# Performance work log

Measured on AMD Instinct MI355X. Metric: run time of the kernel, lower is better.

The kernel has to match this reference:

```python
import jax, jax.numpy as jnp
import numpy as np

N, E, CIN, A, C, NB, B = 20000, 100000, 64, 32, 256, 4, 128
FD = C * NB  # fusion_dims = channels + c_growth*(n_blocks_out-1) with c_growth==channels
HID = 1024


def setup_inputs() -> dict:
    key = jax.random.key(0)
    ks = jax.random.split(key, 24)
    s = 0.05
    inp = {
        "x": jax.random.normal(ks[0], (N, CIN), jnp.float32),
        "edges": jax.random.randint(ks[1], (2, E), 0, N, jnp.int32),
        "edge_weights": jax.random.uniform(ks[2], (E,), jnp.float32),
        "edge_attrs": jax.random.normal(ks[3], (E, A), jnp.float32),
        "bbox_idx": jax.random.randint(ks[4], (N,), 0, B, jnp.int32),
        "num_boxes": B,
        # head GraphConv params: message MLP on [x_dst, x_src-x_dst, edge_attr]
        "W_msg0": jax.random.normal(ks[5], (2 * CIN + A, C), jnp.float32) * s,
        "b_msg0": jnp.zeros((C,), jnp.float32),
        "W_sup0": jax.random.normal(ks[6], (C + CIN, C), jnp.float32) * s,
        "b_sup0": jnp.zeros((C,), jnp.float32),
        # ResBlock params (n_blocks-1 blocks)
        "W_msg": jax.random.normal(ks[7], (NB - 1, 2 * C + A, C), jnp.float32) * s,
        "b_msg": jnp.zeros((NB - 1, C), jnp.float32),
        "W_sup": jax.random.normal(ks[8], (NB - 1, 2 * C, C), jnp.float32) * s,
        "b_sup": jnp.zeros((NB - 1, C), jnp.float32),
        # fusion MLPs [fusion_dims -> 1024]
        "W_fuse": jax.random.normal(ks[9], (FD, HID), jnp.float32) * s,
        "b_fuse": jnp.zeros((HID,), jnp.float32),
        "W_fuse_sup": jax.random.normal(ks[10], (FD, HID), jnp.float32) * s,
        "b_fuse_sup": jnp.zeros((HID,), jnp.float32),
    }
    return inp


def reference(x, edge_weights, edge_attrs, W_msg0, b_msg0, W_sup0, b_sup0,
              W_msg, b_msg, W_sup, b_sup, W_fuse, b_fuse, W_fuse_sup, b_fuse_sup,
              edges, bbox_idx, num_boxes):
    src, dst = edges[0], edges[1]
    n = x.shape[0]

    def gconv(f_in, Wm, bm):
        # per-edge message on [f_dst, f_src - f_dst, edge_attr], weighted sum-aggregate to dst
        h = jnp.concatenate([f_in[dst], f_in[src] - f_in[dst], edge_attrs], axis=1)
        m = jax.nn.relu(h @ Wm + bm) * edge_weights[:, None]
        return jax.ops.segment_sum(m, dst, num_segments=n)

    def super_node(f, x_node, Ws, bs):
        return jax.nn.relu(jnp.concatenate([f, x_node], axis=1) @ Ws + bs)

    # head GraphConv
    f = gconv(x, W_msg0, b_msg0)
    fs = super_node(f, x, W_sup0, b_sup0)
    feats, feats_super = [f], [fs]
    # ResBlocks: residual on node features, fresh super features
    for i in range(NB - 1):
        f = gconv(feats[-1], W_msg[i], b_msg[i]) + feats[-1]
        fs = super_node(f, feats_super[-1], W_sup[i], b_sup[i])
        feats.append(f)
        feats_super.append(fs)

    # n_blocks_out == n_blocks -> take all blocks
    feats_cat = jnp.concatenate(feats, axis=1)            # [N, FD]
    fusion = jax.nn.relu(feats_cat @ W_fuse + b_fuse)     # [N, 1024]
    out_feat = jnp.concatenate([fusion, feats_cat], axis=1)

    fs_cat = jnp.concatenate(feats_super, axis=1)         # [N, FD]
    sums = jax.ops.segment_sum(fs_cat, bbox_idx, num_segments=num_boxes)
    cnts = jax.ops.segment_sum(jnp.ones((n, 1), fs_cat.dtype), bbox_idx, num_segments=num_boxes)
    fs_mean = sums / jnp.maximum(cnts, 1.0)               # scatter(reduce='mean')
    fusion_sup = jax.nn.relu(fs_mean @ W_fuse_sup + b_fuse_sup)
    out_feat_super = jnp.concatenate([fusion_sup, fs_mean], axis=1)
    return out_feat, out_feat_super
```

## Files before the change

kernel.cpp:

```cpp
#include <hip/hip_runtime.h>

#define N_NODES 20000
#define N_EDGES 100000
#define CIN     64
#define A_DIM   32
#define CCH     256
#define NBOX    128
#define FD      1024
#define HID     1024
#define OUT_STRIDE 2048

typedef __attribute__((ext_vector_type(8))) short          short8;
typedef __attribute__((ext_vector_type(8))) unsigned short ushort8;
typedef __attribute__((ext_vector_type(4))) unsigned short ushort4v;
typedef __attribute__((ext_vector_type(4))) float          floatx4;

__device__ __forceinline__ unsigned short f2bf(float f) {
    unsigned int u = __float_as_uint(f);
    u += 0x7fff + ((u >> 16) & 1);
    return (unsigned short)(u >> 16);
}
__device__ __forceinline__ float bf2f(unsigned short h) {
    return __uint_as_float(((unsigned int)h) << 16);
}

__device__ __forceinline__ void glds16(const unsigned short* g, unsigned short* l) {
    __builtin_amdgcn_global_load_lds(
        (const __attribute__((address_space(1))) unsigned int*)g,
        (__attribute__((address_space(3))) unsigned int*)l,
        16, 0, 0);
}

__global__ __launch_bounds__(256) void mfma_dense(
    const unsigned short* __restrict__ src0b, int s0, int o0, int C0,
    const int* __restrict__ ridx0,
    const unsigned short* __restrict__ src1b, int s1, int o1,
    const unsigned short* __restrict__ Wt, const float* __restrict__ bias,
    int do_relu,
    float* __restrict__ outf, int sof, int oof,
    unsigned short* __restrict__ outb, int sob, int oob, int rmode,
    int M, int K, int nbc)
{
    __shared__ __align__(16) unsigned short SM[2][4096];

    const int tid  = threadIdx.x;

    const int nwg  = gridDim.x;
    const int q8   = nwg >> 3, r8 = nwg & 7;
    const int xcd  = blockIdx.x & 7, boff = blockIdx.x >> 3;
    const int bid  = (xcd < r8 ? xcd * (q8 + 1)
                               : r8 * (q8 + 1) + (xcd - r8) * q8) + boff;

    const int rb   = bid / nbc, cb = bid % nbc;
    const int r0   = rb * 128, c0 = cb * 128;
    const int wave = tid >> 6, lane = tid & 63;
    const int quad = lane >> 4, l16 = lane & 15;
    const int wm   = (wave & 1) * 64, wn = (wave >> 1) * 64;

    int arow[2], grow[2], brow[2], kch[2];
    #pragma unroll
    for (int i = 0; i < 2; ++i) {
        const int g  = i * 256 + tid;
        const int rr = g >> 2;
        kch[i] = (g & 3) << 3;
        int gr2 = r0 + rr;
        if (gr2 >= M) gr2 = M - 1;
        grow[i] = gr2;
        arow[i] = ridx0 ? ridx0[gr2] : gr2;
        brow[i] = c0 + rr;
    }
    unsigned short* AsW = &SM[0][wave * 512];
    unsigned short* BsW = &SM[1][wave * 512];

    floatx4 acc[4][4];
    #pragma unroll
    for (int i = 0; i < 4; ++i)
        #pragma unroll
        for (int j = 0; j < 4; ++j) acc[i][j] = (floatx4){0.f, 0.f, 0.f, 0.f};

    for (int k0 = 0; k0 < K; k0 += 32) {
        #pragma unroll
        for (int i = 0; i < 2; ++i) {
            const int kk = k0 + kch[i];
            const unsigned short* ga = (kk < C0)
                ? src0b + (long)arow[i] * s0 + o0 + kk
                : src1b + (long)grow[i] * s1 + o1 + (kk - C0);
            glds16(ga, AsW + i * 2048);
            glds16(Wt + (long)brow[i] * K + k0 + kch[i], BsW + i * 2048);
        }
        __syncthreads();

        short8 af[4], bfr[4];
        #pragma unroll
        for (int mt = 0; mt < 4; ++mt)
            af[mt] = *(const short8*)(&SM[0][(wm + mt * 16 + l16) * 32 + quad * 8]);
        #pragma unroll
        for (int nt = 0; nt < 4; ++nt)
            bfr[nt] = *(const short8*)(&SM[1][(wn + nt * 16 + l16) * 32 + quad * 8]);
        #pragma unroll
        for (int mt = 0; mt < 4; ++mt)
            #pragma unroll
            for (int nt = 0; nt < 4; ++nt)
                acc[mt][nt] = __builtin_amdgcn_mfma_f32_16x16x32_bf16(
                    af[mt], bfr[nt], acc[mt][nt], 0, 0, 0);
        __syncthreads();
    }

    if (outf) {
        #pragma unroll
        for (int nt = 0; nt < 4; ++nt) {
            const int gc = c0 + wn + nt * 16 + l16;
            const float bv = bias ? bias[gc] : 0.f;
            #pragma unroll
            for (int mt = 0; mt < 4; ++mt) {
                #pragma unroll
                for (int reg = 0; reg < 4; ++reg) {
                    const int grr = r0 + wm + mt * 16 + quad * 4 + reg;
                    if (grr < M) {
                        float v = acc[mt][nt][reg] + bv;
                        if (do_relu) v = fmaxf(v, 0.f);
                        outf[(long)grr * sof + oof + gc] = v;
                    }
                }
            }
        }
    }
    if (outb) {
        unsigned short* Cs = &SM[0][0];
        #pragma unroll
        for (int p = 0; p < 2; ++p) {
            if (wm == p * 64) {
                #pragma unroll
                for (int nt = 0; nt < 4; ++nt) {
                    const int col = wn + nt * 16 + l16;
                    const float bv = bias ? bias[c0 + col] : 0.f;
                    #pragma unroll
                    for (int mt = 0; mt < 4; ++mt) {
                        #pragma unroll
                        for (int reg = 0; reg < 4; ++reg) {
                            float v = acc[mt][nt][reg] + bv;
                            if (do_relu) v = fmaxf(v, 0.f);
                            Cs[(mt * 16 + quad * 4 + reg) * 128 + col] = f2bf(v);
                        }
                    }
                }
            }
            __syncthreads();
            const int rl  = tid >> 2;
            const int cc0 = (tid & 3) << 3;
            const int grr2 = r0 + p * 64 + rl;
            if (grr2 < M) {
                const long rowbase = (rmode == 2)
                    ? ((long)(c0 >> 8) * ((long)N_EDGES * 256)
                       + (long)grr2 * 256 + (c0 & 255))
                    : ((long)grr2 * sob + oob + c0);
                #pragma unroll
                for (int j = 0; j < 4; ++j)
                    *(ushort8*)(outb + rowbase + cc0 + j * 32) =
                        *(const ushort8*)(&Cs[rl * 128 + cc0 + j * 32]);
            }
            __syncthreads();
        }
    }
}

__global__ void f32_to_bf16(const float* __restrict__ in,
                            unsigned short* __restrict__ out, int n4) {
    int i = blockIdx.x * blockDim.x + threadIdx.x;
    if (i < n4) {
        float4 v = ((const float4*)in)[i];
        ushort4v h = (ushort4v){f2bf(v.x), f2bf(v.y), f2bf(v.z), f2bf(v.w)};
        ((ushort4v*)out)[i] = h;
    }
}

__global__ __launch_bounds__(256) void agg_kernel(
    const unsigned short* __restrict__ pq,
    const int* __restrict__ rowptr,
    const int* __restrict__ ssrc,
    const float* __restrict__ sew,
    const unsigned short* __restrict__ Rb,
    const float* __restrict__ resid,
    const float* __restrict__ bias,
    float* __restrict__ out, int fofs, int rofs,
    unsigned short* __restrict__ nfbf, int nofs)
{
    const int wid  = (blockIdx.x * blockDim.x + threadIdx.x) >> 6;
    const int lane = threadIdx.x & 63;
    if (wid >= N_NODES) return;
    const int c = lane * 4;

    const ushort4v p4 = *(const ushort4v*)(pq + (long)wid * 512 + c);
    const float4 bb = *(const float4*)(bias + c);
    float pb[4] = {bf2f(p4[0]) + bb.x, bf2f(p4[1]) + bb.y,
                   bf2f(p4[2]) + bb.z, bf2f(p4[3]) + bb.w};
    float acc[4] = {0.f, 0.f, 0.f, 0.f};

    int s = rowptr[wid];
    const int sEnd = rowptr[wid + 1];

    ushort4v q4n, r4n;
    float wn_ = 0.f;
    if (s < sEnd) {
        const int srcn = ssrc[s];
        wn_ = sew[s];
        q4n = *(const ushort4v*)(pq + (long)srcn * 512 + 256 + c);
        r4n = *(const ushort4v*)(Rb + (long)s * 256 + c);
    }
    while (s < sEnd) {
        const ushort4v q4 = q4n, r4 = r4n;
        const float wgt = wn_;
        ++s;
        if (s < sEnd) {
            const int srcn = ssrc[s];
            wn_ = sew[s];
            q4n = *(const ushort4v*)(pq + (long)srcn * 512 + 256 + c);
            r4n = *(const ushort4v*)(Rb + (long)s * 256 + c);
        }
        #pragma unroll
        for (int j = 0; j < 4; ++j)
            acc[j] += fmaxf(pb[j] + bf2f(q4[j]) + bf2f(r4[j]), 0.f) * wgt;
    }
    if (rofs >= 0) {
        const float4 f4 = *(const float4*)(resid + (long)wid * OUT_STRIDE + rofs + c);
        acc[0] += f4.x; acc[1] += f4.y; acc[2] += f4.z; acc[3] += f4.w;
    }
    float4 o; o.x = acc[0]; o.y = acc[1]; o.z = acc[2]; o.w = acc[3];
    *(float4*)(out + (long)wid * OUT_STRIDE + fofs + c) = o;
    ushort4v hb = (ushort4v){f2bf(acc[0]), f2bf(acc[1]), f2bf(acc[2]), f2bf(acc[3])};
    *(ushort4v*)(nfbf + (long)wid * FD + nofs + c) = hb;
}

__global__ void wpq_prep(const float* __restrict__ W, unsigned short* __restrict__ Wpq, int F) {
    int i = blockIdx.x * blockDim.x + threadIdx.x;
    if (i < 512 * F) {
        int nn = i / F, k = i % F;
        float v = (nn < 256) ? (W[k * 256 + nn] - W[(F + k) * 256 + nn])
                             : W[(F + k) * 256 + (nn - 256)];
        Wpq[(long)nn * F + k] = f2bf(v);
    }
}

__global__ __launch_bounds__(256) void wpq_prep3_tiled(
    const float* __restrict__ W, unsigned short* __restrict__ Wpq)
{
    __shared__ float tile[32][33];
    const float* Wi = W + (long)blockIdx.y * 544 * 256;
    unsigned short* Wo = Wpq + (long)blockIdx.y * 512 * 256;
    const int nbx = 16;
    const int n0 = (blockIdx.x % nbx) << 5;
    const int k0 = (blockIdx.x / nbx) << 5;
    const int tx = threadIdx.x & 31, ty = threadIdx.x >> 5;
    #pragma unroll
    for (int r = 0; r < 4; ++r) {
        const int k = k0 + ty + r * 8;
        float v;
        if (n0 < 256)
            v = Wi[(long)k * 256 + n0 + tx] - Wi[(long)(256 + k) * 256 + n0 + tx];
        else
            v = Wi[(long)(256 + k) * 256 + (n0 - 256) + tx];
        tile[ty + r * 8][tx] = v;
    }
    __syncthreads();
    #pragma unroll
    for (int r = 0; r < 4; ++r)
        Wo[(long)(n0 + ty + r * 8) * 256 + k0 + tx] = f2bf(tile[tx][ty + r * 8]);
}

__global__ __launch_bounds__(256) void transpose_tiled(
    const float* __restrict__ in, unsigned short* __restrict__ out,
    int K, int N, long istride, long ostride)
{
    __shared__ float tile[32][33];
    const float* inp = in + (long)blockIdx.y * istride;
    unsigned short* outp = out + (long)blockIdx.y * ostride;
    const int nbx = N >> 5;
    const int n0 = (blockIdx.x % nbx) << 5;
    const int k0 = (blockIdx.x / nbx) << 5;
    const int tx = threadIdx.x & 31, ty = threadIdx.x >> 5;
    #pragma unroll
    for (int r = 0; r < 4; ++r)
        tile[ty + r * 8][tx] = inp[(long)(k0 + ty + r * 8) * N + n0 + tx];
    __syncthreads();
    #pragma unroll
    for (int r = 0; r < 4; ++r)
        outp[(long)(n0 + ty + r * 8) * K + k0 + tx] = f2bf(tile[tx][ty + r * 8]);
}

__global__ void wtr_prep(const float* __restrict__ W_msg0,
                         const float* __restrict__ W_msg,
                         unsigned short* __restrict__ wtr) {
    const int j = blockIdx.y;
    const float* Wi = (j == 0) ? (W_msg0 + 2 * CIN * 256)
                               : (W_msg + (long)(j - 1) * 544 * 256 + 2 * CCH * 256);
    unsigned short* Wo = wtr + (long)j * 256 * 32;
    int i = blockIdx.x * blockDim.x + threadIdx.x;
    if (i < 32 * 256) {
        int k = i / 256, n = i % 256;
        Wo[(long)n * 32 + k] = f2bf(Wi[i]);
    }
}

__global__ void zero_int(int* p, int n) {
    int i = blockIdx.x * blockDim.x + threadIdx.x;
    if (i < n) p[i] = 0;
}
__global__ void hist_kernel(const int* __restrict__ keys, int n, int* __restrict__ cnt) {
    int i = blockIdx.x * blockDim.x + threadIdx.x;
    if (i < n) atomicAdd(&cnt[keys[i]], 1);
}
__global__ __launch_bounds__(1024) void scan_kernel(const int* __restrict__ cnt,
                                                    int* __restrict__ rowptr,
                                                    int* __restrict__ ofs, int n) {
    __shared__ int part[1024];
    const int tid = threadIdx.x;
    const int chunk = (n + 1023) >> 10;
    int s = 0;
    for (int j = 0; j < chunk; ++j) {
        int i = tid * chunk + j;
        if (i < n) s += cnt[i];
    }
    part[tid] = s; __syncthreads();
    for (int d = 1; d < 1024; d <<= 1) {
        int v = (tid >= d) ? part[tid - d] : 0;
        __syncthreads();
        part[tid] += v;
        __syncthreads();
    }
    int run = (tid > 0) ? part[tid - 1] : 0;
    for (int j = 0; j < chunk; ++j) {
        int i = tid * chunk + j;
        if (i < n) { rowptr[i] = run; ofs[i] = run; run += cnt[i]; }
    }
    if (tid == 1023) rowptr[n] = part[1023];
}
__global__ void scatter_edges(const int* __restrict__ src, const int* __restrict__ dst,
                              const float* __restrict__ ew, int* __restrict__ ofs,
                              int* __restrict__ ssrc, float* __restrict__ sew,
                              int* __restrict__ seid) {
    int e = blockIdx.x * blockDim.x + threadIdx.x;
    if (e < N_EDGES) {
        int pos = atomicAdd(&ofs[dst[e]], 1);
        ssrc[pos] = src[e];
        sew[pos]  = ew[e];
        seid[pos] = e;
    }
}
__global__ void scatter_box(const int* __restrict__ bbox, int* __restrict__ ofs,
                            int* __restrict__ snode) {
    int i = blockIdx.x * blockDim.x + threadIdx.x;
    if (i < N_NODES) {
        int pos = atomicAdd(&ofs[bbox[i]], 1);
        snode[pos] = i;
    }
}

__global__ __launch_bounds__(256) void box_mean_csr(
    const unsigned short* __restrict__ fsbf, const int* __restrict__ bptr,
    const int* __restrict__ snode, float* __restrict__ out_super,
    unsigned short* __restrict__ fsmeanb)
{
    const int b = blockIdx.x >> 2;
    const int c = ((blockIdx.x & 3) << 8) + threadIdx.x;
    const int s0 = bptr[b], s1 = bptr[b + 1];
    float sum = 0.f;
    for (int s = s0; s < s1; ++s)
        sum += bf2f(fsbf[(long)snode[s] * FD + c]);
    const float mean = sum / fmaxf((float)(s1 - s0), 1.f);
    out_super[(long)b * OUT_STRIDE + HID + c] = mean;
    fsmeanb[(long)b * FD + c] = f2bf(mean);
}

extern "C" void kernel_launch(void* const* d_in, const int* in_sizes, int n_in,
                              void* d_out, int out_size, void* d_ws, size_t ws_size,
                              hipStream_t stream) {
    const float* x      = (const float*)d_in[0];
    const int*   edges  = (const int*)d_in[1];
    const float* ew     = (const float*)d_in[2];
    const float* ea     = (const float*)d_in[3];
    const int*   bbox   = (const int*)d_in[4];
    const float* W_msg0 = (const float*)d_in[6];
    const float* b_msg0 = (const float*)d_in[7];
    const float* W_sup0 = (const float*)d_in[8];
    const float* b_sup0 = (const float*)d_in[9];
    const float* W_msg  = (const float*)d_in[10];
    const float* b_msg  = (const float*)d_in[11];
    const float* W_sup  = (const float*)d_in[12];
    const float* b_sup  = (const float*)d_in[13];
    const float* W_fuse = (const float*)d_in[14];
    const float* b_fuse = (const float*)d_in[15];
    const float* W_fsup = (const float*)d_in[16];
    const float* b_fsup = (const float*)d_in[17];

    float* out       = (float*)d_out;
    float* out_super = out + (long)N_NODES * OUT_STRIDE;

    char* w = (char*)d_ws;
    auto alloc = [&](size_t bytes) { char* p = w; w += (bytes + 63) & ~63ULL; return p; };
    unsigned short* fsbf    = (unsigned short*)alloc((size_t)N_NODES * FD * 2);
    unsigned short* nfbf    = (unsigned short*)alloc((size_t)N_NODES * FD * 2);
    unsigned short* pq      = (unsigned short*)alloc((size_t)N_NODES * 512 * 2);
    unsigned short* xb      = (unsigned short*)alloc((size_t)N_NODES * CIN * 2);
    unsigned short* eab     = (unsigned short*)alloc((size_t)N_EDGES * A_DIM * 2);
    unsigned short* Rb4     = (unsigned short*)alloc((size_t)N_EDGES * 1024 * 2);
    unsigned short* wpq0    = (unsigned short*)alloc((size_t)512 * CIN * 2);
    unsigned short* wpq     = (unsigned short*)alloc((size_t)3 * 512 * CCH * 2);
    unsigned short* wtr     = (unsigned short*)alloc((size_t)4 * 256 * 32 * 2);
    unsigned short* wt_sup0 = (unsigned short*)alloc((size_t)256 * 320 * 2);
    unsigned short* wt_sup  = (unsigned short*)alloc((size_t)3 * 256 * 512 * 2);
    unsigned short* wt_fuse = (unsigned short*)alloc((size_t)1024 * 1024 * 2);
    unsigned short* wt_fsup = (unsigned short*)alloc((size_t)1024 * 1024 * 2);
    unsigned short* fsmeanb = (unsigned short*)alloc((size_t)NBOX * FD * 2);
    float* sew        = (float*)alloc((size_t)N_EDGES * 4);
    int* cnt          = (int*)alloc((size_t)(N_NODES + 1) * 4);
    int* rowptr       = (int*)alloc((size_t)(N_NODES + 1) * 4);
    int* ofs          = (int*)alloc((size_t)(N_NODES + 1) * 4);
    int* ssrc         = (int*)alloc((size_t)N_EDGES * 4);
    int* seid         = (int*)alloc((size_t)N_EDGES * 4);
    int* bcnt         = (int*)alloc(129 * 4);
    int* bptr         = (int*)alloc(129 * 4);
    int* bofs         = (int*)alloc(129 * 4);
    int* snode        = (int*)alloc((size_t)N_NODES * 4);

    const int* srcp = edges;
    const int* dstp = edges + N_EDGES;

    f32_to_bf16<<<(N_NODES * CIN / 4 + 255) / 256, 256, 0, stream>>>(x, xb, N_NODES * CIN / 4);
    f32_to_bf16<<<(N_EDGES * A_DIM / 4 + 255) / 256, 256, 0, stream>>>(ea, eab, N_EDGES * A_DIM / 4);

    wpq_prep<<<(512 * CIN + 255) / 256, 256, 0, stream>>>(W_msg0, wpq0, CIN);
    wpq_prep3_tiled<<<dim3(128, 3), 256, 0, stream>>>(W_msg, wpq);
    wtr_prep<<<dim3((32 * 256 + 255) / 256, 4), 256, 0, stream>>>(W_msg0, W_msg, wtr);
    transpose_tiled<<<dim3(80, 1),   256, 0, stream>>>(W_sup0, wt_sup0, 320, 256, 0, 0);
    transpose_tiled<<<dim3(128, 3),  256, 0, stream>>>(W_sup,  wt_sup,  512, 256,
                                                       512 * 256, 256 * 512);
    transpose_tiled<<<dim3(1024, 1), 256, 0, stream>>>(W_fuse, wt_fuse, 1024, 1024, 0, 0);
    transpose_tiled<<<dim3(1024, 1), 256, 0, stream>>>(W_fsup, wt_fsup, 1024, 1024, 0, 0);

    zero_int<<<(N_NODES + 256) / 256, 256, 0, stream>>>(cnt, N_NODES + 1);
    zero_int<<<1, 256, 0, stream>>>(bcnt, 129);
    hist_kernel<<<(N_EDGES + 255) / 256, 256, 0, stream>>>(dstp, N_EDGES, cnt);
    hist_kernel<<<(N_NODES + 255) / 256, 256, 0, stream>>>(bbox, N_NODES, bcnt);
    scan_kernel<<<1, 1024, 0, stream>>>(cnt, rowptr, ofs, N_NODES);
    scan_kernel<<<1, 1024, 0, stream>>>(bcnt, bptr, bofs, NBOX);
    scatter_edges<<<(N_EDGES + 255) / 256, 256, 0, stream>>>(srcp, dstp, ew, ofs, ssrc, sew, seid);
    scatter_box<<<(N_NODES + 255) / 256, 256, 0, stream>>>(bbox, bofs, snode);

    const int GRB = (N_NODES + 127) / 128;
    const int GEB = (N_EDGES + 127) / 128;

    mfma_dense<<<GEB * 8, 256, 0, stream>>>(eab, A_DIM, 0, A_DIM, seid,
        nullptr, 0, 0, wtr, nullptr, 0,
        nullptr, 0, 0, Rb4, 0, 0, 2, N_EDGES, A_DIM, 8);

    const long RLS = (long)N_EDGES * 256;

    mfma_dense<<<GRB * 4, 256, 0, stream>>>(xb, CIN, 0, CIN, nullptr,
        nullptr, 0, 0, wpq0, nullptr, 0,
        nullptr, 0, 0, pq, 512, 0, 0, N_NODES, CIN, 4);
    agg_kernel<<<(N_NODES + 3) / 4, 256, 0, stream>>>(pq, rowptr, ssrc, sew,
        Rb4, out, b_msg0, out, HID, -1, nfbf, 0);
    mfma_dense<<<GRB * 2, 256, 0, stream>>>(nfbf, FD, 0, CCH, nullptr,
        xb, CIN, 0, wt_sup0, b_sup0, 1,
        nullptr, 0, 0, fsbf, FD, 0, 0, N_NODES, CCH + CIN, 2);

    for (int i = 0; i < 3; ++i) {
        const int fi = HID + CCH * i, fo = HID + CCH * (i + 1);
        mfma_dense<<<GRB * 4, 256, 0, stream>>>(nfbf, FD, CCH * i, CCH, nullptr,
            nullptr, 0, 0, wpq + (long)i * 512 * CCH, nullptr, 0,
            nullptr, 0, 0, pq, 512, 0, 0, N_NODES, CCH, 4);
        agg_kernel<<<(N_NODES + 3) / 4, 256, 0, stream>>>(pq, rowptr, ssrc, sew,
            Rb4 + (long)(i + 1) * RLS, out, b_msg + i * CCH,
            out, fo, fi, nfbf, CCH * (i + 1));
        mfma_dense<<<GRB * 2, 256, 0, stream>>>(nfbf, FD, CCH * (i + 1), CCH, nullptr,
            fsbf, FD, CCH * i, wt_sup + (long)i * 256 * 512, b_sup + i * CCH, 1,
            nullptr, 0, 0, fsbf, FD, CCH * (i + 1), 0, N_NODES, 2 * CCH, 2);
    }

    mfma_dense<<<GRB * 8, 256, 0, stream>>>(nfbf, FD, 0, FD, nullptr,
        nullptr, 0, 0, wt_fuse, b_fuse, 1,
        out, OUT_STRIDE, 0, nullptr, 0, 0, 0, N_NODES, FD, 8);

    box_mean_csr<<<NBOX * 4, 256, 0, stream>>>(fsbf, bptr, snode, out_super, fsmeanb);
    mfma_dense<<<8, 256, 0, stream>>>(fsmeanb, FD, 0, FD, nullptr,
        nullptr, 0, 0, wt_fsup, b_fsup, 1,
        out_super, OUT_STRIDE, 0, nullptr, 0, 0, 0, NBOX, FD, 8);
}
```

Measured before the change: 858.4 us.

## Batch independent GEMMs into shared grids and merge prep kernels

```diff
diff --git a/kernel.cpp b/kernel.cpp
--- a/kernel.cpp
+++ b/kernel.cpp
@@ -31,25 +31,48 @@
         16, 0, 0);
 }
 
-__global__ __launch_bounds__(256) void mfma_dense(
-    const unsigned short* __restrict__ src0b, int s0, int o0, int C0,
-    const int* __restrict__ ridx0,
-    const unsigned short* __restrict__ src1b, int s1, int o1,
-    const unsigned short* __restrict__ Wt, const float* __restrict__ bias,
-    int do_relu,
-    float* __restrict__ outf, int sof, int oof,
-    unsigned short* __restrict__ outb, int sob, int oob, int rmode,
-    int M, int K, int nbc)
+struct GD {
+    const unsigned short* src0b;
+    const unsigned short* src1b;
+    const unsigned short* Wt;
+    const float* bias;
+    const int* ridx0;
+    float* outf;
+    unsigned short* outb;
+    int s0, o0, C0, s1, o1, do_relu, sof, oof, sob, oob, rmode, M, K, nbc;
+};
+
+__global__ __launch_bounds__(256) void mfma_dense(GD A, GD B, int n0)
 {
     __shared__ __align__(16) unsigned short SM[2][4096];
 
-    const int tid  = threadIdx.x;
-
-    const int nwg  = gridDim.x;
-    const int q8   = nwg >> 3, r8 = nwg & 7;
-    const int xcd  = blockIdx.x & 7, boff = blockIdx.x >> 3;
-    const int bid  = (xcd < r8 ? xcd * (q8 + 1)
-                               : r8 * (q8 + 1) + (xcd - r8) * q8) + boff;
+    const int tid = threadIdx.x;
+    const bool fa = (int)blockIdx.x < n0;
+
+    const unsigned short* src0b = fa ? A.src0b : B.src0b;
+    const unsigned short* src1b = fa ? A.src1b : B.src1b;
+    const unsigned short* Wt    = fa ? A.Wt    : B.Wt;
+    const float* bias           = fa ? A.bias  : B.bias;
+    const int*   ridx0          = fa ? A.ridx0 : B.ridx0;
+    float* outf                 = fa ? A.outf  : B.outf;
+    unsigned short* outb        = fa ? A.outb  : B.outb;
+    const int s0  = fa ? A.s0  : B.s0,  o0  = fa ? A.o0  : B.o0;
+    const int C0  = fa ? A.C0  : B.C0;
+    const int s1  = fa ? A.s1  : B.s1,  o1  = fa ? A.o1  : B.o1;
+    const int do_relu = fa ? A.do_relu : B.do_relu;
+    const int sof = fa ? A.sof : B.sof, oof = fa ? A.oof : B.oof;
+    const int sob = fa ? A.sob : B.sob, oob = fa ? A.oob : B.oob;
+    const int rmode = fa ? A.rmode : B.rmode;
+    const int M   = fa ? A.M   : B.M;
+    const int K   = fa ? A.K   : B.K;
+    const int nbc = fa ? A.nbc : B.nbc;
+
+    const int nwg = fa ? n0 : (int)gridDim.x - n0;
+    const int lb  = (int)blockIdx.x - (fa ? 0 : n0);
+    const int q8  = nwg >> 3, r8 = nwg & 7;
+    const int xcd = lb & 7, boff = lb >> 3;
+    const int bid = (xcd < r8 ? xcd * (q8 + 1)
+                              : r8 * (q8 + 1) + (xcd - r8) * q8) + boff;
 
     const int rb   = bid / nbc, cb = bid % nbc;
     const int r0   = rb * 128, c0 = cb * 128;
@@ -164,16 +187,6 @@
     }
 }
 
-__global__ void f32_to_bf16(const float* __restrict__ in,
-                            unsigned short* __restrict__ out, int n4) {
-    int i = blockIdx.x * blockDim.x + threadIdx.x;
-    if (i < n4) {
-        float4 v = ((const float4*)in)[i];
-        ushort4v h = (ushort4v){f2bf(v.x), f2bf(v.y), f2bf(v.z), f2bf(v.w)};
-        ((ushort4v*)out)[i] = h;
-    }
-}
-
 __global__ __launch_bounds__(256) void agg_kernel(
     const unsigned short* __restrict__ pq,
     const int* __restrict__ rowptr,
@@ -231,53 +244,14 @@
     *(ushort4v*)(nfbf + (long)wid * FD + nofs + c) = hb;
 }
 
-__global__ void wpq_prep(const float* __restrict__ W, unsigned short* __restrict__ Wpq, int F) {
-    int i = blockIdx.x * blockDim.x + threadIdx.x;
-    if (i < 512 * F) {
-        int nn = i / F, k = i % F;
-        float v = (nn < 256) ? (W[k * 256 + nn] - W[(F + k) * 256 + nn])
-                             : W[(F + k) * 256 + (nn - 256)];
-        Wpq[(long)nn * F + k] = f2bf(v);
-    }
-}
-
-__global__ __launch_bounds__(256) void wpq_prep3_tiled(
-    const float* __restrict__ W, unsigned short* __restrict__ Wpq)
+__device__ __forceinline__ void tr_block(const float* inp, unsigned short* outp,
+                                         int K, int N, int bidx, int tid,
+                                         float (*tile)[33])
 {
-    __shared__ float tile[32][33];
-    const float* Wi = W + (long)blockIdx.y * 544 * 256;
-    unsigned short* Wo = Wpq + (long)blockIdx.y * 512 * 256;
-    const int nbx = 16;
-    const int n0 = (blockIdx.x % nbx) << 5;
-    const int k0 = (blockIdx.x / nbx) << 5;
-    const int tx = threadIdx.x & 31, ty = threadIdx.x >> 5;
-    #pragma unroll
-    for (int r = 0; r < 4; ++r) {
-        const int k = k0 + ty + r * 8;
-        float v;
-        if (n0 < 256)
-            v = Wi[(long)k * 256 + n0 + tx] - Wi[(long)(256 + k) * 256 + n0 + tx];
-        else
-            v = Wi[(long)(256 + k) * 256 + (n0 - 256) + tx];
-        tile[ty + r * 8][tx] = v;
-    }
-    __syncthreads();
-    #pragma unroll
-    for (int r = 0; r < 4; ++r)
-        Wo[(long)(n0 + ty + r * 8) * 256 + k0 + tx] = f2bf(tile[tx][ty + r * 8]);
-}
-
-__global__ __launch_bounds__(256) void transpose_tiled(
-    const float* __restrict__ in, unsigned short* __restrict__ out,
-    int K, int N, long istride, long ostride)
-{
-    __shared__ float tile[32][33];
-    const float* inp = in + (long)blockIdx.y * istride;
-    unsigned short* outp = out + (long)blockIdx.y * ostride;
     const int nbx = N >> 5;
-    const int n0 = (blockIdx.x % nbx) << 5;
-    const int k0 = (blockIdx.x / nbx) << 5;
-    const int tx = threadIdx.x & 31, ty = threadIdx.x >> 5;
+    const int n0 = (bidx % nbx) << 5;
+    const int k0 = (bidx / nbx) << 5;
+    const int tx = tid & 31, ty = tid >> 5;
     #pragma unroll
     for (int r = 0; r < 4; ++r)
         tile[ty + r * 8][tx] = inp[(long)(k0 + ty + r * 8) * N + n0 + tx];
@@ -287,38 +261,129 @@
         outp[(long)(n0 + ty + r * 8) * K + k0 + tx] = f2bf(tile[tx][ty + r * 8]);
 }
 
-__global__ void wtr_prep(const float* __restrict__ W_msg0,
-                         const float* __restrict__ W_msg,
-                         unsigned short* __restrict__ wtr) {
-    const int j = blockIdx.y;
-    const float* Wi = (j == 0) ? (W_msg0 + 2 * CIN * 256)
-                               : (W_msg + (long)(j - 1) * 544 * 256 + 2 * CCH * 256);
-    unsigned short* Wo = wtr + (long)j * 256 * 32;
+#define PB_CVTX  1250
+#define PB_CVTE  3125
+#define PB_WPQ0  128
+#define PB_WPQ3  384
+#define PB_WTR   128
+#define PB_TS0   80
+#define PB_TS3   384
+#define PB_TF    1024
+#define PREP_BLOCKS (PB_CVTX+PB_CVTE+PB_WPQ0+PB_WPQ3+PB_WTR+PB_TS0+PB_TS3+PB_TF+PB_TF)
+
+__global__ __launch_bounds__(256) void prep_all(
+    const float* __restrict__ x, const float* __restrict__ ea,
+    const float* __restrict__ W_msg0, const float* __restrict__ W_msg,
+    const float* __restrict__ W_sup0, const float* __restrict__ W_sup,
+    const float* __restrict__ W_fuse, const float* __restrict__ W_fsup,
+    unsigned short* __restrict__ xb, unsigned short* __restrict__ eab,
+    unsigned short* __restrict__ wpq0, unsigned short* __restrict__ wpq,
+    unsigned short* __restrict__ wtr,
+    unsigned short* __restrict__ wt_sup0, unsigned short* __restrict__ wt_sup,
+    unsigned short* __restrict__ wt_fuse, unsigned short* __restrict__ wt_fsup)
+{
+    __shared__ float tile[32][33];
+    const int tid = threadIdx.x;
+    int b = blockIdx.x;
+
+    if (b < PB_CVTX) {
+        int i = b * 256 + tid;
+        float4 v = ((const float4*)x)[i];
+        ((ushort4v*)xb)[i] = (ushort4v){f2bf(v.x), f2bf(v.y), f2bf(v.z), f2bf(v.w)};
+        return;
+    }
+    b -= PB_CVTX;
+    if (b < PB_CVTE) {
+        int i = b * 256 + tid;
+        float4 v = ((const float4*)ea)[i];
+        ((ushort4v*)eab)[i] = (ushort4v){f2bf(v.x), f2bf(v.y), f2bf(v.z), f2bf(v.w)};
+        return;
+    }
+    b -= PB_CVTE;
+    if (b < PB_WPQ0) {
+        int i = b * 256 + tid;
+        int nn = i >> 6, k = i & 63;
+        float v = (nn < 256) ? (W_msg0[k * 256 + nn] - W_msg0[(64 + k) * 256 + nn])
+                             : (W_msg0[(64 + k) * 256 + (nn - 256)]);
+        wpq0[(long)nn * 64 + k] = f2bf(v);
+        return;
+    }
+    b -= PB_WPQ0;
+    if (b < PB_WPQ3) {
+        const int slab = b / 128, bb = b % 128;
+        const float* Wi = W_msg + (long)slab * 544 * 256;
+        unsigned short* Wo = wpq + (long)slab * 512 * 256;
+        const int n0 = (bb & 15) << 5;
+        const int k0 = (bb >> 4) << 5;
+        const int tx = tid & 31, ty = tid >> 5;
+        #pragma unroll
+        for (int r = 0; r < 4; ++r) {
+            const int k = k0 + ty + r * 8;
+            float v;
+            if (n0 < 256)
+                v = Wi[(long)k * 256 + n0 + tx] - Wi[(long)(256 + k) * 256 + n0 + tx];
+            else
+                v = Wi[(long)(256 + k) * 256 + (n0 - 256) + tx];
+            tile[ty + r * 8][tx] = v;
+        }
+        __syncthreads();
+        #pragma unroll
+        for (int r = 0; r < 4; ++r)
+            Wo[(long)(n0 + ty + r * 8) * 256 + k0 + tx] = f2bf(tile[tx][ty + r * 8]);
+        return;
+    }
+    b -= PB_WPQ3;
+    if (b < PB_WTR) {
+        const int j = b >> 5;
+        const float* Wi = (j == 0) ? (W_msg0 + 2 * CIN * 256)
+                                   : (W_msg + (long)(j - 1) * 544 * 256 + 2 * CCH * 256);
+        unsigned short* Wo = wtr + (long)j * 256 * 32;
+        int i = (b & 31) * 256 + tid;
+        int k = i >> 8, n = i & 255;
+        Wo[(long)n * 32 + k] = f2bf(Wi[i]);
+        return;
+    }
+    b -= PB_WTR;
+    if (b < PB_TS0) { tr_block(W_sup0, wt_sup0, 320, 256, b, tid, tile); return; }
+    b -= PB_TS0;
+    if (b < PB_TS3) {
+        const int slab = b / 128;
+        tr_block(W_sup + (long)slab * 512 * 256, wt_sup + (long)slab * 256 * 512,
+                 512, 256, b % 128, tid, tile);
+        return;
+    }
+    b -= PB_TS3;
+    if (b < PB_TF) { tr_block(W_fuse, wt_fuse, 1024, 1024, b, tid, tile); return; }
+    b -= PB_TF;
+    tr_block(W_fsup, wt_fsup, 1024, 1024, b, tid, tile);
+}
+
+__global__ void zero2(int* __restrict__ cnt, int* __restrict__ bcnt) {
     int i = blockIdx.x * blockDim.x + threadIdx.x;
-    if (i < 32 * 256) {
-        int k = i / 256, n = i % 256;
-        Wo[(long)n * 32 + k] = f2bf(Wi[i]);
-    }
-}
-
-__global__ void zero_int(int* p, int n) {
+    if (i < N_NODES + 1) cnt[i] = 0;
+    else if (i - (N_NODES + 1) < 129) bcnt[i - (N_NODES + 1)] = 0;
+}
+__global__ void hist2(const int* __restrict__ dst, const int* __restrict__ bbox,
+                      int* __restrict__ cnt, int* __restrict__ bcnt) {
     int i = blockIdx.x * blockDim.x + threadIdx.x;
-    if (i < n) p[i] = 0;
-}
-__global__ void hist_kernel(const int* __restrict__ keys, int n, int* __restrict__ cnt) {
-    int i = blockIdx.x * blockDim.x + threadIdx.x;
-    if (i < n) atomicAdd(&cnt[keys[i]], 1);
-}
-__global__ __launch_bounds__(1024) void scan_kernel(const int* __restrict__ cnt,
-                                                    int* __restrict__ rowptr,
-                                                    int* __restrict__ ofs, int n) {
+    if (i < N_EDGES) atomicAdd(&cnt[dst[i]], 1);
+    else if (i - N_EDGES < N_NODES) atomicAdd(&bcnt[bbox[i - N_EDGES]], 1);
+}
+__global__ __launch_bounds__(1024) void scan2(
+    const int* __restrict__ cnt,  int* __restrict__ rowptr, int* __restrict__ ofs,
+    const int* __restrict__ bcnt, int* __restrict__ bptr,   int* __restrict__ bofs)
+{
     __shared__ int part[1024];
     const int tid = threadIdx.x;
+    const int n = blockIdx.x == 0 ? N_NODES : NBOX;
+    const int* c   = blockIdx.x == 0 ? cnt    : bcnt;
+    int* rp        = blockIdx.x == 0 ? rowptr : bptr;
+    int* op        = blockIdx.x == 0 ? ofs    : bofs;
     const int chunk = (n + 1023) >> 10;
     int s = 0;
     for (int j = 0; j < chunk; ++j) {
         int i = tid * chunk + j;
-        if (i < n) s += cnt[i];
+        if (i < n) s += c[i];
     }
     part[tid] = s; __syncthreads();
     for (int d = 1; d < 1024; d <<= 1) {
@@ -330,28 +395,26 @@
     int run = (tid > 0) ? part[tid - 1] : 0;
     for (int j = 0; j < chunk; ++j) {
         int i = tid * chunk + j;
-        if (i < n) { rowptr[i] = run; ofs[i] = run; run += cnt[i]; }
-    }
-    if (tid == 1023) rowptr[n] = part[1023];
-}
-__global__ void scatter_edges(const int* __restrict__ src, const int* __restrict__ dst,
-                              const float* __restrict__ ew, int* __restrict__ ofs,
-                              int* __restrict__ ssrc, float* __restrict__ sew,
-                              int* __restrict__ seid) {
-    int e = blockIdx.x * blockDim.x + threadIdx.x;
-    if (e < N_EDGES) {
-        int pos = atomicAdd(&ofs[dst[e]], 1);
-        ssrc[pos] = src[e];
-        sew[pos]  = ew[e];
-        seid[pos] = e;
-    }
-}
-__global__ void scatter_box(const int* __restrict__ bbox, int* __restrict__ ofs,
-                            int* __restrict__ snode) {
+        if (i < n) { rp[i] = run; op[i] = run; run += c[i]; }
+    }
+    if (tid == 1023) rp[n] = part[1023];
+}
+__global__ void scatter2(const int* __restrict__ src, const int* __restrict__ dst,
+                         const float* __restrict__ ew, int* __restrict__ ofs,
+                         int* __restrict__ ssrc, float* __restrict__ sew,
+                         int* __restrict__ seid,
+                         const int* __restrict__ bbox, int* __restrict__ bofs,
+                         int* __restrict__ snode) {
     int i = blockIdx.x * blockDim.x + threadIdx.x;
-    if (i < N_NODES) {
-        int pos = atomicAdd(&ofs[bbox[i]], 1);
-        snode[pos] = i;
+    if (i < N_EDGES) {
+        int pos = atomicAdd(&ofs[dst[i]], 1);
+        ssrc[pos] = src[i];
+        sew[pos]  = ew[i];
+        seid[pos] = i;
+    } else if (i - N_EDGES < N_NODES) {
+        int j = i - N_EDGES;
+        int pos = atomicAdd(&bofs[bbox[j]], 1);
+        snode[pos] = j;
     }
 }
 
@@ -425,64 +488,76 @@
     const int* srcp = edges;
     const int* dstp = edges + N_EDGES;
 
-    f32_to_bf16<<<(N_NODES * CIN / 4 + 255) / 256, 256, 0, stream>>>(x, xb, N_NODES * CIN / 4);
-    f32_to_bf16<<<(N_EDGES * A_DIM / 4 + 255) / 256, 256, 0, stream>>>(ea, eab, N_EDGES * A_DIM / 4);
-
-    wpq_prep<<<(512 * CIN + 255) / 256, 256, 0, stream>>>(W_msg0, wpq0, CIN);
-    wpq_prep3_tiled<<<dim3(128, 3), 256, 0, stream>>>(W_msg, wpq);
-    wtr_prep<<<dim3((32 * 256 + 255) / 256, 4), 256, 0, stream>>>(W_msg0, W_msg, wtr);
-    transpose_tiled<<<dim3(80, 1),   256, 0, stream>>>(W_sup0, wt_sup0, 320, 256, 0, 0);
-    transpose_tiled<<<dim3(128, 3),  256, 0, stream>>>(W_sup,  wt_sup,  512, 256,
-                                                       512 * 256, 256 * 512);
-    transpose_tiled<<<dim3(1024, 1), 256, 0, stream>>>(W_fuse, wt_fuse, 1024, 1024, 0, 0);
-    transpose_tiled<<<dim3(1024, 1), 256, 0, stream>>>(W_fsup, wt_fsup, 1024, 1024, 0, 0);
-
-    zero_int<<<(N_NODES + 256) / 256, 256, 0, stream>>>(cnt, N_NODES + 1);
-    zero_int<<<1, 256, 0, stream>>>(bcnt, 129);
-    hist_kernel<<<(N_EDGES + 255) / 256, 256, 0, stream>>>(dstp, N_EDGES, cnt);
-    hist_kernel<<<(N_NODES + 255) / 256, 256, 0, stream>>>(bbox, N_NODES, bcnt);
-    scan_kernel<<<1, 1024, 0, stream>>>(cnt, rowptr, ofs, N_NODES);
-    scan_kernel<<<1, 1024, 0, stream>>>(bcnt, bptr, bofs, NBOX);
-    scatter_edges<<<(N_EDGES + 255) / 256, 256, 0, stream>>>(srcp, dstp, ew, ofs, ssrc, sew, seid);
-    scatter_box<<<(N_NODES + 255) / 256, 256, 0, stream>>>(bbox, bofs, snode);
+    prep_all<<<PREP_BLOCKS, 256, 0, stream>>>(
+        x, ea, W_msg0, W_msg, W_sup0, W_sup, W_fuse, W_fsup,
+        xb, eab, wpq0, wpq, wtr, wt_sup0, wt_sup, wt_fuse, wt_fsup);
+
+    zero2<<<(N_NODES + 130 + 255) / 256, 256, 0, stream>>>(cnt, bcnt);
+    hist2<<<(N_EDGES + N_NODES + 255) / 256, 256, 0, stream>>>(dstp, bbox, cnt, bcnt);
+    scan2<<<2, 1024, 0, stream>>>(cnt, rowptr, ofs, bcnt, bptr, bofs);
+    scatter2<<<(N_EDGES + N_NODES + 255) / 256, 256, 0, stream>>>(
+        srcp, dstp, ew, ofs, ssrc, sew, seid, bbox, bofs, snode);
 
     const int GRB = (N_NODES + 127) / 128;
     const int GEB = (N_EDGES + 127) / 128;
-
-    mfma_dense<<<GEB * 8, 256, 0, stream>>>(eab, A_DIM, 0, A_DIM, seid,
-        nullptr, 0, 0, wtr, nullptr, 0,
-        nullptr, 0, 0, Rb4, 0, 0, 2, N_EDGES, A_DIM, 8);
-
     const long RLS = (long)N_EDGES * 256;
 
-    mfma_dense<<<GRB * 4, 256, 0, stream>>>(xb, CIN, 0, CIN, nullptr,
-        nullptr, 0, 0, wpq0, nullptr, 0,
-        nullptr, 0, 0, pq, 512, 0, 0, N_NODES, CIN, 4);
-    agg_kernel<<<(N_NODES + 3) / 4, 256, 0, stream>>>(pq, rowptr, ssrc, sew,
+    auto mk = [](const unsigned short* src0b, int s0, int o0, int C0,
+                 const int* ridx0,
+                 const unsigned short* src1b, int s1, int o1,
+                 const unsigned short* Wt, const float* bias, int relu,
+                 float* outf, int sof, int oof,
+                 unsigned short* outb, int sob, int oob, int rmode,
+                 int M, int K, int nbc) {
+        GD g;
+        g.src0b = src0b; g.s0 = s0; g.o0 = o0; g.C0 = C0;
+        g.ridx0 = ridx0;
+        g.src1b = src1b; g.s1 = s1; g.o1 = o1;
+        g.Wt = Wt; g.bias = bias; g.do_relu = relu;
+        g.outf = outf; g.sof = sof; g.oof = oof;
+        g.outb = outb; g.sob = sob; g.oob = oob; g.rmode = rmode;
+        g.M = M; g.K = K; g.nbc = nbc;
+        return g;
+    };
+
+    GD gR   = mk(eab, A_DIM, 0, A_DIM, seid, nullptr, 0, 0, wtr, nullptr, 0,
+                 nullptr, 0, 0, Rb4, 0, 0, 2, N_EDGES, A_DIM, 8);
+    GD gPQh = mk(xb, CIN, 0, CIN, nullptr, nullptr, 0, 0, wpq0, nullptr, 0,
+                 nullptr, 0, 0, pq, 512, 0, 0, N_NODES, CIN, 4);
+    GD gS0  = mk(nfbf, FD, 0, CCH, nullptr, xb, CIN, 0, wt_sup0, b_sup0, 1,
+                 nullptr, 0, 0, fsbf, FD, 0, 0, N_NODES, CCH + CIN, 2);
+    GD gPQ[3], gS[3];
+    for (int i = 0; i < 3; ++i) {
+        gPQ[i] = mk(nfbf, FD, CCH * i, CCH, nullptr, nullptr, 0, 0,
+                    wpq + (long)i * 512 * CCH, nullptr, 0,
+                    nullptr, 0, 0, pq, 512, 0, 0, N_NODES, CCH, 4);
+        gS[i]  = mk(nfbf, FD, CCH * (i + 1), CCH, nullptr, fsbf, FD, CCH * i,
+                    wt_sup + (long)i * 256 * 512, b_sup + i * CCH, 1,
+                    nullptr, 0, 0, fsbf, FD, CCH * (i + 1), 0, N_NODES, 2 * CCH, 2);
+    }
+    GD gFU  = mk(nfbf, FD, 0, FD, nullptr, nullptr, 0, 0, wt_fuse, b_fuse, 1,
+                 out, OUT_STRIDE, 0, nullptr, 0, 0, 0, N_NODES, FD, 8);
+    GD gFS  = mk(fsmeanb, FD, 0, FD, nullptr, nullptr, 0, 0, wt_fsup, b_fsup, 1,
+                 out_super, OUT_STRIDE, 0, nullptr, 0, 0, 0, NBOX, FD, 8);
+
+    const int AGRID = (N_NODES + 3) / 4;
+
+    mfma_dense<<<GEB * 8 + GRB * 4, 256, 0, stream>>>(gR, gPQh, GEB * 8);
+
+    agg_kernel<<<AGRID, 256, 0, stream>>>(pq, rowptr, ssrc, sew,
         Rb4, out, b_msg0, out, HID, -1, nfbf, 0);
-    mfma_dense<<<GRB * 2, 256, 0, stream>>>(nfbf, FD, 0, CCH, nullptr,
-        xb, CIN, 0, wt_sup0, b_sup0, 1,
-        nullptr, 0, 0, fsbf, FD, 0, 0, N_NODES, CCH + CIN, 2);
-
+
+    mfma_dense<<<GRB * 6, 256, 0, stream>>>(gS0, gPQ[0], GRB * 2);
     for (int i = 0; i < 3; ++i) {
-        const int fi = HID + CCH * i, fo = HID + CCH * (i + 1);
-        mfma_dense<<<GRB * 4, 256, 0, stream>>>(nfbf, FD, CCH * i, CCH, nullptr,
-            nullptr, 0, 0, wpq + (long)i * 512 * CCH, nullptr, 0,
-            nullptr, 0, 0, pq, 512, 0, 0, N_NODES, CCH, 4);
-        agg_kernel<<<(N_NODES + 3) / 4, 256, 0, stream>>>(pq, rowptr, ssrc, sew,
+        agg_kernel<<<AGRID, 256, 0, stream>>>(pq, rowptr, ssrc, sew,
             Rb4 + (long)(i + 1) * RLS, out, b_msg + i * CCH,
-            out, fo, fi, nfbf, CCH * (i + 1));
-        mfma_dense<<<GRB * 2, 256, 0, stream>>>(nfbf, FD, CCH * (i + 1), CCH, nullptr,
-            fsbf, FD, CCH * i, wt_sup + (long)i * 256 * 512, b_sup + i * CCH, 1,
-            nullptr, 0, 0, fsbf, FD, CCH * (i + 1), 0, N_NODES, 2 * CCH, 2);
-    }
-
-    mfma_dense<<<GRB * 8, 256, 0, stream>>>(nfbf, FD, 0, FD, nullptr,
-        nullptr, 0, 0, wt_fuse, b_fuse, 1,
-        out, OUT_STRIDE, 0, nullptr, 0, 0, 0, N_NODES, FD, 8);
+            out, HID + CCH * (i + 1), HID + CCH * i, nfbf, CCH * (i + 1));
+        if (i < 2)
+            mfma_dense<<<GRB * 6, 256, 0, stream>>>(gS[i], gPQ[i + 1], GRB * 2);
+    }
+
+    mfma_dense<<<GRB * 10, 256, 0, stream>>>(gS[2], gFU, GRB * 2);
 
     box_mean_csr<<<NBOX * 4, 256, 0, stream>>>(fsbf, bptr, snode, out_super, fsmeanb);
-    mfma_dense<<<8, 256, 0, stream>>>(fsmeanb, FD, 0, FD, nullptr,
-        nullptr, 0, 0, wt_fsup, b_fsup, 1,
-        out_super, OUT_STRIDE, 0, nullptr, 0, 0, 0, NBOX, FD, 8);
-}
+    mfma_dense<<<8, 256, 0, stream>>>(gFS, gFS, 8);
+}
```

New measurement: 789.1 us. 8.1% less time.
